# Kernel tuning notes

Hardware: AMD Instinct MI355X
Metric: run time of the kernel (lower is better)

Reference implementation:

```python
import jax, jax.numpy as jnp
import numpy as np

N_NODES = 50000
N_EDGES = 800000
IN_DIM = 128
HEADS = 4
OUT_DIM = 16
HD = HEADS * OUT_DIM  # 64
EDGE_DIM = 1
NEG_SLOPE = 0.2


def setup_inputs() -> dict:
    key = jax.random.key(0)
    ks = jax.random.split(key, 12)
    x = jax.random.normal(ks[0], (N_NODES, IN_DIM), dtype=jnp.float32)
    edge_index = jax.random.randint(ks[1], (2, N_EDGES), 0, N_NODES, dtype=jnp.int64)
    edge_attr = jax.random.uniform(ks[2], (N_EDGES, EDGE_DIM), dtype=jnp.float32)
    s = 0.1
    Wl = jax.random.normal(ks[3], (IN_DIM, HD), dtype=jnp.float32) * s
    bl = jax.random.normal(ks[4], (HD,), dtype=jnp.float32) * s
    Wr = jax.random.normal(ks[5], (IN_DIM, HD), dtype=jnp.float32) * s
    br = jax.random.normal(ks[6], (HD,), dtype=jnp.float32) * s
    We = jax.random.normal(ks[7], (EDGE_DIM, HD), dtype=jnp.float32) * s
    att = jax.random.normal(ks[8], (HEADS, OUT_DIM), dtype=jnp.float32) * s
    bias_out = jax.random.normal(ks[9], (HD,), dtype=jnp.float32) * s
    Wres = jax.random.normal(ks[10], (IN_DIM, HD), dtype=jnp.float32) * s
    bres = jax.random.normal(ks[11], (HD,), dtype=jnp.float32) * s
    return {"x": x, "edge_index": edge_index, "edge_attr": edge_attr,
            "Wl": Wl, "bl": bl, "Wr": Wr, "br": br, "We": We,
            "att": att, "bias_out": bias_out, "Wres": Wres, "bres": bres}


def _gatv2_layer(x, edge_index, edge_attr, Wl, bl, Wr, br, We, att, bias_out, Wres, bres):
    src, dst = edge_index[0], edge_index[1]
    # projections: [N, H, D]
    x_l = (x @ Wl + bl).reshape(N_NODES, HEADS, OUT_DIM)
    x_r = (x @ Wr + br).reshape(N_NODES, HEADS, OUT_DIM)
    edge_emb = (edge_attr @ We).reshape(N_EDGES, HEADS, OUT_DIM)
    # per-edge attention score (GATv2): a^T LeakyReLU(x_l[src] + x_r[dst] + e)
    x_j = x_l[src]                                   # [E, H, D] gather (source message)
    feat = x_j + x_r[dst] + edge_emb                 # [E, H, D]
    score = jnp.einsum('ehd,hd->eh', jax.nn.leaky_relu(feat, NEG_SLOPE), att)  # [E, H]
    # segment softmax over destination neighborhoods
    m = jax.ops.segment_max(score, dst, num_segments=N_NODES)   # [N, H]
    ex = jnp.exp(score - m[dst])                                 # [E, H]
    denom = jax.ops.segment_sum(ex, dst, num_segments=N_NODES)  # [N, H]
    alpha = ex / (denom[dst] + 1e-16)                            # [E, H]
    # scatter-add aggregation of weighted source messages
    out = jax.ops.segment_sum(alpha[:, :, None] * x_j, dst, num_segments=N_NODES)  # [N, H, D]
    out = out.reshape(N_NODES, HD) + bias_out        # concat heads + conv bias
    # residual (in_dim != out_features -> linear projection), then ELU
    out = out + (x @ Wres + bres)
    out = jax.nn.elu(out)
    return out, edge_index, alpha


def reference(x, edge_index, edge_attr, Wl, bl, Wr, br, We, att, bias_out, Wres, bres):
    return _gatv2_layer(x, edge_index, edge_attr, Wl, bl, Wr, br, We, att, bias_out, Wres, bres)
```

## Files before the change

### kernel.cpp

```cpp
#include <hip/hip_runtime.h>
#include <math.h>

#define N_NODES 50000
#define N_EDGES 800000
#define IN_DIM  128
#define HEADS   4
#define OUT_DIM 16
#define HD      64
#define NEG_SLOPE 0.2f
#define CAP     128
#define LOG2E   1.44269504088896340736f

__device__ __forceinline__ float hw_exp2(float x) {
    return __builtin_amdgcn_exp2f(x);
}

__global__ __launch_bounds__(256)
void k1_proj(const float* __restrict__ x,
             const float* __restrict__ Wl, const float* __restrict__ bl,
             const float* __restrict__ Wr, const float* __restrict__ br,
             const float* __restrict__ Wres, const float* __restrict__ bres,
             int* __restrict__ count,
             float* __restrict__ xl, float* __restrict__ xr,
             float* __restrict__ xres) {
    __shared__ float xs[16][IN_DIM];
    const int base = blockIdx.x * 16;

    const int gid = blockIdx.x * 256 + threadIdx.x;
    if (gid < N_NODES) count[gid] = 0;

    {
        const float4* s4 = (const float4*)(x + (size_t)base * IN_DIM);
        float4* d4 = (float4*)&xs[0][0];
        for (int i = threadIdx.x; i < 16 * IN_DIM / 4; i += 256) d4[i] = s4[i];
    }
    __syncthreads();

    const int group = threadIdx.x >> 6;
    const int col   = threadIdx.x & 63;

    float al[4] = {0, 0, 0, 0}, ar[4] = {0, 0, 0, 0}, as[4] = {0, 0, 0, 0};
#pragma unroll 8
    for (int k0 = 0; k0 < IN_DIM; k0 += 4) {
        float xv[4][4];
        *(float4*)xv[0] = *(const float4*)&xs[group * 4 + 0][k0];
        *(float4*)xv[1] = *(const float4*)&xs[group * 4 + 1][k0];
        *(float4*)xv[2] = *(const float4*)&xs[group * 4 + 2][k0];
        *(float4*)xv[3] = *(const float4*)&xs[group * 4 + 3][k0];
#pragma unroll
        for (int kk = 0; kk < 4; ++kk) {
            const float wl = Wl[(k0 + kk) * HD + col];
            const float wr = Wr[(k0 + kk) * HD + col];
            const float ws = Wres[(k0 + kk) * HD + col];
#pragma unroll
            for (int i = 0; i < 4; ++i) {
                al[i] += xv[i][kk] * wl;
                ar[i] += xv[i][kk] * wr;
                as[i] += xv[i][kk] * ws;
            }
        }
    }
    const float blv = bl[col], brv = br[col], bsv = bres[col];
    const size_t n0 = (size_t)(base + group * 4) * HD + col;
#pragma unroll
    for (int i = 0; i < 4; ++i) {
        xl[n0 + i * HD]   = al[i] + blv;
        xr[n0 + i * HD]   = ar[i] + brv;
        xres[n0 + i * HD] = as[i] + bsv;
    }
}

__global__ __launch_bounds__(256)
void k2_hist(const int* __restrict__ dst, int* __restrict__ count) {
    int e = blockIdx.x * blockDim.x + threadIdx.x;
    if (e < N_EDGES) atomicAdd(&count[dst[e]], 1);
}

#define SCAN_BLOCKS 196

__global__ __launch_bounds__(256)
void k3a_scan1(const int* __restrict__ count, int* __restrict__ incl,
               int* __restrict__ bsum) {
    __shared__ int s[256];
    const int t = threadIdx.x;
    const int i = blockIdx.x * 256 + t;
    int c = (i < N_NODES) ? count[i] : 0;
    s[t] = c;
    __syncthreads();
    for (int off = 1; off < 256; off <<= 1) {
        int v = (t >= off) ? s[t - off] : 0;
        __syncthreads();
        s[t] += v;
        __syncthreads();
    }
    if (i < N_NODES) incl[i] = s[t];
    if (t == 255) bsum[blockIdx.x] = s[255];
}

__global__ __launch_bounds__(256)
void k3b_scan2(int* __restrict__ bsum, int* __restrict__ boff) {
    __shared__ int s[256];
    const int t = threadIdx.x;
    int c = (t < SCAN_BLOCKS) ? bsum[t] : 0;
    s[t] = c;
    __syncthreads();
    for (int off = 1; off < 256; off <<= 1) {
        int v = (t >= off) ? s[t - off] : 0;
        __syncthreads();
        s[t] += v;
        __syncthreads();
    }
    if (t < SCAN_BLOCKS) boff[t] = s[t] - c;
}

__global__ __launch_bounds__(256)
void k3c_scan3(const int* __restrict__ count, int* __restrict__ incl ,
               const int* __restrict__ boff, int* __restrict__ cursor) {
    const int i = blockIdx.x * 256 + threadIdx.x;
    if (i >= N_NODES) return;
    const int v = incl[i] - count[i] + boff[blockIdx.x];
    incl[i] = v;
    cursor[i] = v;
}

__global__ __launch_bounds__(256)
void k4_scatter(const int* __restrict__ src, const int* __restrict__ dst,
                const float* __restrict__ ea,
                int* __restrict__ cursor, int4* __restrict__ recs,
                float* __restrict__ out_ei) {
    int e = blockIdx.x * blockDim.x + threadIdx.x;
    if (e >= N_EDGES) return;
    const int d = dst[e];
    const int s = src[e];
    const int pos = atomicAdd(&cursor[d], 1);
    recs[pos] = make_int4(e, s, __float_as_int(ea[e]), 0);
    out_ei[e] = (float)s;
    out_ei[N_EDGES + e] = (float)d;
}

__global__ __launch_bounds__(256)
void k5_node(const int4* __restrict__ recs,
             const int* __restrict__ rowptr, const int* __restrict__ count,
             const float* __restrict__ xl, const float* __restrict__ xr,
             const float* __restrict__ xres,
             const float* __restrict__ We, const float* __restrict__ att,
             const float* __restrict__ bias_out,
             float* __restrict__ out, float* __restrict__ out_alpha) {
    __shared__ float sc_lds[4][CAP][HEADS];

    const int wv   = threadIdx.x >> 6;
    const int lane = threadIdx.x & 63;
    const int u    = lane & 15;
    const int g    = lane >> 4;
    const int n    = blockIdx.x * 4 + wv;

    const int base = rowptr[n];
    const int deg  = count[n];

    const float4 xr4 = *(const float4*)(xr  + (size_t)n * HD + 4 * u);
    const float4 We4 = *(const float4*)(We  + 4 * u);
    float4 at4       = *(const float4*)(att + 4 * u);
    at4.x *= LOG2E; at4.y *= LOG2E; at4.z *= LOG2E; at4.w *= LOG2E;

    float m = -INFINITY, dsum = 0.f;
    float4 acc = make_float4(0.f, 0.f, 0.f, 0.f);

    for (int c0 = 0; c0 < deg; c0 += 64) {
        const int nrem = min(64, deg - c0);
        int s_my = 0; float a_my = 0.f;
        if (lane < nrem) {
            const int4 r = recs[base + c0 + lane];
            s_my = r.y;
            a_my = __int_as_float(r.z);
        }
        const int nchunk = (nrem + 3) >> 2;

        int   j   = g;
        bool  v   = j < nrem;
        int   s   = __shfl(s_my, j);
        float aev = __shfl(a_my, j);
        float4 xlv = make_float4(0.f, 0.f, 0.f, 0.f);
        if (v) xlv = *(const float4*)(xl + (size_t)s * HD + 4 * u);

        for (int c = 0; c < nchunk; ++c) {
            const float4 cur  = xlv;
            const bool   curv = v;
            const float  ca   = aev;
            const int    cj   = 4 * c + g;
            j = 4 * (c + 1) + g;
            v = j < nrem;
            s   = __shfl(s_my, j & 63);
            aev = __shfl(a_my, j & 63);
            if (v) xlv = *(const float4*)(xl + (size_t)s * HD + 4 * u);

            if (curv) {
                float f0 = cur.x + xr4.x + ca * We4.x;
                float f1 = cur.y + xr4.y + ca * We4.y;
                float f2 = cur.z + xr4.z + ca * We4.z;
                float f3 = cur.w + xr4.w + ca * We4.w;
                f0 = f0 > 0.f ? f0 : NEG_SLOPE * f0;
                f1 = f1 > 0.f ? f1 : NEG_SLOPE * f1;
                f2 = f2 > 0.f ? f2 : NEG_SLOPE * f2;
                f3 = f3 > 0.f ? f3 : NEG_SLOPE * f3;
                float p = f0 * at4.x + f1 * at4.y + f2 * at4.z + f3 * at4.w;
                p += __shfl_xor(p, 1);
                p += __shfl_xor(p, 2);
                const int jj = c0 + cj;
                if (jj < CAP && (u & 3) == 0) sc_lds[wv][jj][u >> 2] = p;
                const float t    = hw_exp2(-fabsf(p - m));
                const bool  up   = (p >= m);
                const float scl  = up ? t : 1.f;
                const float pe   = up ? 1.f : t;
                m = fmaxf(m, p);
                dsum  = dsum * scl + pe;
                acc.x = acc.x * scl + pe * cur.x;
                acc.y = acc.y * scl + pe * cur.y;
                acc.z = acc.z * scl + pe * cur.z;
                acc.w = acc.w * scl + pe * cur.w;
            }
        }
    }

#pragma unroll
    for (int off = 16; off <= 32; off <<= 1) {
        const float mo = __shfl_xor(m, off);
        const float d2 = __shfl_xor(dsum, off);
        float4 a2;
        a2.x = __shfl_xor(acc.x, off);
        a2.y = __shfl_xor(acc.y, off);
        a2.z = __shfl_xor(acc.z, off);
        a2.w = __shfl_xor(acc.w, off);
        const float mm = fmaxf(m, mo);
        const float s1 = (m  == -INFINITY) ? 0.f : hw_exp2(m - mm);
        const float s2 = (mo == -INFINITY) ? 0.f : hw_exp2(mo - mm);
        dsum  = dsum * s1 + d2 * s2;
        acc.x = acc.x * s1 + a2.x * s2;
        acc.y = acc.y * s1 + a2.y * s2;
        acc.z = acc.z * s1 + a2.z * s2;
        acc.w = acc.w * s1 + a2.w * s2;
        m = mm;
    }
    const float inv = 1.f / (dsum + 1e-16f);

    const float m0 = __shfl(m, 0),  m1 = __shfl(m, 4);
    const float m2 = __shfl(m, 8),  m3 = __shfl(m, 12);
    const float i0 = __shfl(inv, 0), i1 = __shfl(inv, 4);
    const float i2 = __shfl(inv, 8), i3 = __shfl(inv, 12);

    __syncthreads();

    for (int jj = lane; jj < deg; jj += 64) {
        const int4 r = recs[base + jj];
        const int  e = r.x;
        float s0, s1, s2, s3;
        if (jj < CAP) {
            const float4 sc4 = *(const float4*)&sc_lds[wv][jj][0];
            s0 = sc4.x; s1 = sc4.y; s2 = sc4.z; s3 = sc4.w;
        } else {
            const int   sN  = r.y;
            const float aev = __int_as_float(r.z);
            float sc[4];
            for (int h2 = 0; h2 < 4; ++h2) {
                float a2 = 0.f;
                for (int d2 = 0; d2 < 16; ++d2) {
                    const int hd2 = h2 * 16 + d2;
                    float f = xl[(size_t)sN * HD + hd2] + xr[(size_t)n * HD + hd2]
                              + aev * We[hd2];
                    f = f > 0.f ? f : NEG_SLOPE * f;
                    a2 += f * att[hd2];
                }
                sc[h2] = a2 * LOG2E;
            }
            s0 = sc[0]; s1 = sc[1]; s2 = sc[2]; s3 = sc[3];
        }
        float4 a4;
        a4.x = hw_exp2(s0 - m0) * i0;
        a4.y = hw_exp2(s1 - m1) * i1;
        a4.z = hw_exp2(s2 - m2) * i2;
        a4.w = hw_exp2(s3 - m3) * i3;
        *(float4*)(out_alpha + (size_t)e * HEADS) = a4;
    }

    if (g == 0) {
        const float4 xs4 = *(const float4*)(xres + (size_t)n * HD + 4 * u);
        const float4 b4  = *(const float4*)(bias_out + 4 * u);
        float4 o;
        o.x = acc.x * inv + b4.x + xs4.x;
        o.y = acc.y * inv + b4.y + xs4.y;
        o.z = acc.z * inv + b4.z + xs4.z;
        o.w = acc.w * inv + b4.w + xs4.w;
        o.x = o.x > 0.f ? o.x : __expf(o.x) - 1.f;
        o.y = o.y > 0.f ? o.y : __expf(o.y) - 1.f;
        o.z = o.z > 0.f ? o.z : __expf(o.z) - 1.f;
        o.w = o.w > 0.f ? o.w : __expf(o.w) - 1.f;
        *(float4*)(out + (size_t)n * HD + 4 * u) = o;
    }
}

extern "C" void kernel_launch(void* const* d_in, const int* in_sizes, int n_in,
                              void* d_out, int out_size, void* d_ws, size_t ws_size,
                              hipStream_t stream) {
    const float* x        = (const float*)d_in[0];
    const int*   ei       = (const int*)d_in[1];
    const float* ea       = (const float*)d_in[2];
    const float* Wl       = (const float*)d_in[3];
    const float* bl       = (const float*)d_in[4];
    const float* Wr       = (const float*)d_in[5];
    const float* br       = (const float*)d_in[6];
    const float* We       = (const float*)d_in[7];
    const float* att      = (const float*)d_in[8];
    const float* bias_out = (const float*)d_in[9];
    const float* Wres     = (const float*)d_in[10];
    const float* bres     = (const float*)d_in[11];

    const int* src = ei;
    const int* dst = ei + N_EDGES;

    float* out       = (float*)d_out;
    float* out_ei    = out + (size_t)N_NODES * HD;
    float* out_alpha = out_ei + 2 * (size_t)N_EDGES;

    float* ws   = (float*)d_ws;
    float* xl   = ws;
    float* xr   = xl + (size_t)N_NODES * HD;
    float* xres = xr + (size_t)N_NODES * HD;
    int* ibuf   = (int*)(xres + (size_t)N_NODES * HD);
    int* count  = ibuf;
    int* rowptr = count + N_NODES;
    int* cursor = rowptr + N_NODES;
    int* bsum   = cursor + N_NODES;
    int* boff   = bsum + SCAN_BLOCKS;
    size_t recoff = (size_t)(boff + SCAN_BLOCKS - (int*)d_ws);
    recoff = (recoff + 3) & ~(size_t)3;
    int4* recs  = (int4*)((int*)d_ws + recoff);

    k1_proj<<<N_NODES / 16, 256, 0, stream>>>(x, Wl, bl, Wr, br, Wres, bres,
                                              count, xl, xr, xres);
    k2_hist<<<N_EDGES / 256, 256, 0, stream>>>(dst, count);
    k3a_scan1<<<SCAN_BLOCKS, 256, 0, stream>>>(count, rowptr, bsum);
    k3b_scan2<<<1, 256, 0, stream>>>(bsum, boff);
    k3c_scan3<<<SCAN_BLOCKS, 256, 0, stream>>>(count, rowptr, boff, cursor);
    k4_scatter<<<(N_EDGES + 255) / 256, 256, 0, stream>>>(src, dst, ea, cursor,
                                                          recs, out_ei);
    k5_node<<<N_NODES / 4, 256, 0, stream>>>(recs, rowptr, count,
                                             xl, xr, xres, We, att, bias_out,
                                             out, out_alpha);
}
```

Baseline: 328.5 us.

## Register-tile projection GEMM with transposed LDS tile and split-K shuffle reduction

Reworks the node projection kernel to handle 32 nodes per block. The x tile is stored transposed in LDS, and each thread accumulates an 8-node by 4-column tile for all three weight matrices using float4 weight loads. The K dimension is split across four lane groups and combined with cross-lane shuffle reductions. The aim is more reuse per weight and LDS load and vectorized stores, at the cost of higher register pressure and extra shuffle work.

```diff
diff --git a/kernel.cpp b/kernel.cpp
--- a/kernel.cpp
+++ b/kernel.cpp
@@ -23,50 +23,101 @@
              int* __restrict__ count,
              float* __restrict__ xl, float* __restrict__ xr,
              float* __restrict__ xres) {
-    __shared__ float xs[16][IN_DIM];
-    const int base = blockIdx.x * 16;
+    __shared__ float xsT[IN_DIM][36];
+    const int base = blockIdx.x * 32;
 
     const int gid = blockIdx.x * 256 + threadIdx.x;
     if (gid < N_NODES) count[gid] = 0;
 
     {
-        const float4* s4 = (const float4*)(x + (size_t)base * IN_DIM);
-        float4* d4 = (float4*)&xs[0][0];
-        for (int i = threadIdx.x; i < 16 * IN_DIM / 4; i += 256) d4[i] = s4[i];
+        const float4* x4 = (const float4*)x;
+#pragma unroll
+        for (int r = 0; r < 4; ++r) {
+            const int E    = threadIdx.x * 4 + r;
+            const int node = E >> 5;
+            const int kq   = E & 31;
+            float4 v = make_float4(0.f, 0.f, 0.f, 0.f);
+            if (base + node < N_NODES) v = x4[(size_t)(base + node) * 32 + kq];
+            xsT[4 * kq + 0][node] = v.x;
+            xsT[4 * kq + 1][node] = v.y;
+            xsT[4 * kq + 2][node] = v.z;
+            xsT[4 * kq + 3][node] = v.w;
+        }
     }
     __syncthreads();
 
-    const int group = threadIdx.x >> 6;
-    const int col   = threadIdx.x & 63;
-
-    float al[4] = {0, 0, 0, 0}, ar[4] = {0, 0, 0, 0}, as[4] = {0, 0, 0, 0};
-#pragma unroll 8
+    const int lane = threadIdx.x & 63;
+    const int wv   = threadIdx.x >> 6;
+    const int u    = lane & 15;
+    const int g    = lane >> 4;
+    const int n0   = wv * 8;
+
+    float4 aL[8], aR[8], aS[8];
+#pragma unroll
+    for (int i = 0; i < 8; ++i) {
+        aL[i] = make_float4(0.f, 0.f, 0.f, 0.f);
+        aR[i] = make_float4(0.f, 0.f, 0.f, 0.f);
+        aS[i] = make_float4(0.f, 0.f, 0.f, 0.f);
+    }
+
+    const float* pL = Wl   + g * HD + 4 * u;
+    const float* pR = Wr   + g * HD + 4 * u;
+    const float* pS = Wres + g * HD + 4 * u;
+
+#pragma unroll 2
     for (int k0 = 0; k0 < IN_DIM; k0 += 4) {
-        float xv[4][4];
-        *(float4*)xv[0] = *(const float4*)&xs[group * 4 + 0][k0];
-        *(float4*)xv[1] = *(const float4*)&xs[group * 4 + 1][k0];
-        *(float4*)xv[2] = *(const float4*)&xs[group * 4 + 2][k0];
-        *(float4*)xv[3] = *(const float4*)&xs[group * 4 + 3][k0];
-#pragma unroll
-        for (int kk = 0; kk < 4; ++kk) {
-            const float wl = Wl[(k0 + kk) * HD + col];
-            const float wr = Wr[(k0 + kk) * HD + col];
-            const float ws = Wres[(k0 + kk) * HD + col];
-#pragma unroll
-            for (int i = 0; i < 4; ++i) {
-                al[i] += xv[i][kk] * wl;
-                ar[i] += xv[i][kk] * wr;
-                as[i] += xv[i][kk] * ws;
+        const int k = k0 + g;
+        const float4 wl4 = *(const float4*)(pL + k0 * HD);
+        const float4 wr4 = *(const float4*)(pR + k0 * HD);
+        const float4 ws4 = *(const float4*)(pS + k0 * HD);
+        const float4 xa  = *(const float4*)&xsT[k][n0];
+        const float4 xb  = *(const float4*)&xsT[k][n0 + 4];
+        const float xn[8] = {xa.x, xa.y, xa.z, xa.w, xb.x, xb.y, xb.z, xb.w};
+#pragma unroll
+        for (int i = 0; i < 8; ++i) {
+            aL[i].x += xn[i] * wl4.x; aL[i].y += xn[i] * wl4.y;
+            aL[i].z += xn[i] * wl4.z; aL[i].w += xn[i] * wl4.w;
+            aR[i].x += xn[i] * wr4.x; aR[i].y += xn[i] * wr4.y;
+            aR[i].z += xn[i] * wr4.z; aR[i].w += xn[i] * wr4.w;
+            aS[i].x += xn[i] * ws4.x; aS[i].y += xn[i] * ws4.y;
+            aS[i].z += xn[i] * ws4.z; aS[i].w += xn[i] * ws4.w;
+        }
+    }
+
+#pragma unroll
+    for (int off = 16; off <= 32; off <<= 1) {
+#pragma unroll
+        for (int i = 0; i < 8; ++i) {
+            aL[i].x += __shfl_xor(aL[i].x, off); aL[i].y += __shfl_xor(aL[i].y, off);
+            aL[i].z += __shfl_xor(aL[i].z, off); aL[i].w += __shfl_xor(aL[i].w, off);
+            aR[i].x += __shfl_xor(aR[i].x, off); aR[i].y += __shfl_xor(aR[i].y, off);
+            aR[i].z += __shfl_xor(aR[i].z, off); aR[i].w += __shfl_xor(aR[i].w, off);
+            aS[i].x += __shfl_xor(aS[i].x, off); aS[i].y += __shfl_xor(aS[i].y, off);
+            aS[i].z += __shfl_xor(aS[i].z, off); aS[i].w += __shfl_xor(aS[i].w, off);
+        }
+    }
+
+    if (g == 0) {
+        const float4 bl4 = *(const float4*)(bl   + 4 * u);
+        const float4 br4 = *(const float4*)(br   + 4 * u);
+        const float4 bs4 = *(const float4*)(bres + 4 * u);
+#pragma unroll
+        for (int i = 0; i < 8; ++i) {
+            const int node = base + n0 + i;
+            if (node < N_NODES) {
+                float4 o;
+                const size_t off0 = (size_t)node * HD + 4 * u;
+                o.x = aL[i].x + bl4.x; o.y = aL[i].y + bl4.y;
+                o.z = aL[i].z + bl4.z; o.w = aL[i].w + bl4.w;
+                *(float4*)(xl + off0) = o;
+                o.x = aR[i].x + br4.x; o.y = aR[i].y + br4.y;
+                o.z = aR[i].z + br4.z; o.w = aR[i].w + br4.w;
+                *(float4*)(xr + off0) = o;
+                o.x = aS[i].x + bs4.x; o.y = aS[i].y + bs4.y;
+                o.z = aS[i].z + bs4.z; o.w = aS[i].w + bs4.w;
+                *(float4*)(xres + off0) = o;
             }
         }
-    }
-    const float blv = bl[col], brv = br[col], bsv = bres[col];
-    const size_t n0 = (size_t)(base + group * 4) * HD + col;
-#pragma unroll
-    for (int i = 0; i < 4; ++i) {
-        xl[n0 + i * HD]   = al[i] + blv;
-        xr[n0 + i * HD]   = ar[i] + brv;
-        xres[n0 + i * HD] = as[i] + bsv;
     }
 }
 
@@ -334,8 +385,8 @@
     recoff = (recoff + 3) & ~(size_t)3;
     int4* recs  = (int4*)((int*)d_ws + recoff);
 
-    k1_proj<<<N_NODES / 16, 256, 0, stream>>>(x, Wl, bl, Wr, br, Wres, bres,
-                                              count, xl, xr, xres);
+    k1_proj<<<(N_NODES + 31) / 32, 256, 0, stream>>>(x, Wl, bl, Wr, br, Wres, bres,
+                                                     count, xl, xr, xres);
     k2_hist<<<N_EDGES / 256, 256, 0, stream>>>(dst, count);
     k3a_scan1<<<SCAN_BLOCKS, 256, 0, stream>>>(count, rowptr, bsum);
     k3b_scan2<<<1, 256, 0, stream>>>(bsum, boff);
```

Measured after the change: 317.6 us. 1.03x faster.
